# Kernel optimization log

Measured on AMD Instinct MI355X. Metric: run time of the kernel, lower is better.

## Reference

```python
import jax, jax.numpy as jnp
import numpy as np

T, B, I, H, L = 512, 256, 128, 256, 2

def _gru_layer(x, W_ih, W_hh, b_ih, b_hh):
    # x: [T, B, in], W_ih: [3H, in], W_hh: [3H, H], biases: [3H]
    # PyTorch gate order: r, z, n
    Hd = W_hh.shape[1]
    gi = jnp.einsum('tbi,gi->tbg', x, W_ih) + b_ih  # precompute input gates [T,B,3H]

    def step(h, gi_t):
        gh = h @ W_hh.T + b_hh
        i_r, i_z, i_n = jnp.split(gi_t, 3, axis=-1)
        h_r, h_z, h_n = jnp.split(gh, 3, axis=-1)
        r = jax.nn.sigmoid(i_r + h_r)
        z = jax.nn.sigmoid(i_z + h_z)
        n = jnp.tanh(i_n + r * h_n)
        h_new = (1.0 - z) * n + z * h
        return h_new, h_new

    h0 = jnp.zeros((x.shape[1], Hd), dtype=x.dtype)
    _, hs = jax.lax.scan(step, h0, gi)
    return hs  # [T, B, H]

def setup_inputs() -> dict:
    key = jax.random.key(0)
    ks = jax.random.split(key, 11)
    s = 1.0 / np.sqrt(H)
    u = lambda k, shp: jax.random.uniform(k, shp, jnp.float32, -s, s)
    return {
        'x': jax.random.normal(ks[0], (T, B, I), jnp.float32),
        'W_ih0': u(ks[1], (3 * H, I)),
        'W_hh0': u(ks[2], (3 * H, H)),
        'b_ih0': u(ks[3], (3 * H,)),
        'b_hh0': u(ks[4], (3 * H,)),
        'W_ih1': u(ks[5], (3 * H, H)),
        'W_hh1': u(ks[6], (3 * H, H)),
        'b_ih1': u(ks[7], (3 * H,)),
        'b_hh1': u(ks[8], (3 * H,)),
        'W_fc': u(ks[9], (H, H)),
        'b_fc': u(ks[10], (H,)),
    }

def reference(x, W_ih0, W_hh0, b_ih0, b_hh0, W_ih1, W_hh1, b_ih1, b_hh1, W_fc, b_fc):
    h1 = _gru_layer(x, W_ih0, W_hh0, b_ih0, b_hh0)   # [T,B,H]
    h2 = _gru_layer(h1, W_ih1, W_hh1, b_ih1, b_hh1)  # [T,B,H]
    last = h2[-1]                                    # [B,H] last timestep
    return last @ W_fc.T + b_fc
```

## Files before the change

### kernel.cpp

```cpp
#include <hip/hip_runtime.h>

#define TT 512
#define BB 256
#define II 128
#define HH 256

typedef __attribute__((ext_vector_type(8))) short short8;
typedef __attribute__((ext_vector_type(4))) float floatx4;
typedef __attribute__((ext_vector_type(4))) float fvec4;
typedef unsigned long long u64;

#define OFF_WIH0 0
#define OFF_WHH0 (OFF_WIH0 + 3 * HH * II)
#define OFF_WIH1 (OFF_WHH0 + 3 * HH * HH)
#define OFF_WHH1 (OFF_WIH1 + 3 * HH * HH)
#define W_TOTAL (OFF_WHH1 + 3 * HH * HH)
#define H1G_OFF W_TOTAL
#define H2G_OFF (H1G_OFF + 2 * BB * HH)
#define WS_SHORTS (H2G_OFF + 2 * BB * HH)
#define FLAGS_OFF_BYTES (WS_SHORTS * 2)
#define FLAG_STRIDE 32
#define HPARW (BB * HH / 4)

struct U64x2 { u64 lo, hi; };

__device__ __forceinline__ short f2bf(float f) {
  unsigned u = __builtin_bit_cast(unsigned, f);
  u = u + 0x7fffu + ((u >> 16) & 1u);
  return (short)(u >> 16);
}
__device__ __forceinline__ float fast_sigmoid(float x) {
  return __fdividef(1.0f, 1.0f + __expf(-x));
}
__device__ __forceinline__ float fast_tanh(float x) {
  return 1.0f - __fdividef(2.0f, 1.0f + __expf(2.0f * x));
}
__device__ __forceinline__ short8 cvt8(const float* __restrict__ p) {
  fvec4 lo = *(const fvec4*)p;
  fvec4 hi = *(const fvec4*)(p + 4);
  short8 r;
  r[0] = f2bf(lo[0]); r[1] = f2bf(lo[1]); r[2] = f2bf(lo[2]); r[3] = f2bf(lo[3]);
  r[4] = f2bf(hi[0]); r[5] = f2bf(hi[1]); r[6] = f2bf(hi[2]); r[7] = f2bf(hi[3]);
  return r;
}
__device__ __forceinline__ u64 ld_sc1(const u64* p) {
  return __hip_atomic_load(p, __ATOMIC_RELAXED, __HIP_MEMORY_SCOPE_AGENT);
}
__device__ __forceinline__ unsigned ld_flag(const unsigned* p) {
  return __hip_atomic_load(p, __ATOMIC_RELAXED, __HIP_MEMORY_SCOPE_AGENT);
}
__device__ __forceinline__ void st_flag(unsigned* p, unsigned v) {
  __hip_atomic_store(p, v, __ATOMIC_RELAXED, __HIP_MEMORY_SCOPE_AGENT);
}
__device__ __forceinline__ void st_h(unsigned short* p, unsigned short v) {
  __hip_atomic_store(p, v, __ATOMIC_RELAXED, __HIP_MEMORY_SCOPE_AGENT);
}
#define DRAIN_VMEM asm volatile("s_waitcnt vmcnt(0)" ::: "memory")

__global__ __launch_bounds__(256) void cvt_weights(
    const float* __restrict__ w0, const float* __restrict__ w1,
    const float* __restrict__ w2, const float* __restrict__ w3,
    short* __restrict__ out) {
  int i = blockIdx.x * 256 + threadIdx.x;
  if (i >= W_TOTAL) return;
  float v;
  if (i < OFF_WHH0)      v = w0[i - OFF_WIH0];
  else if (i < OFF_WIH1) v = w1[i - OFF_WHH0];
  else if (i < OFF_WHH1) v = w2[i - OFF_WIH1];
  else                   v = w3[i - OFF_WHH1];
  out[i] = f2bf(v);
}

__global__ __launch_bounds__(256) void init_state(unsigned* __restrict__ hz,
                                                  unsigned* __restrict__ flags) {
  int i = blockIdx.x * 256 + threadIdx.x;
  if (i < 2 * BB * HH) hz[i] = 0u;
  if (i < 32 * FLAG_STRIDE) flags[i] = 0u;
}

__global__ __launch_bounds__(64) void gru_sync(
    const float* __restrict__ x, const short* __restrict__ wb,
    const float* __restrict__ bih0, const float* __restrict__ bhh0,
    const float* __restrict__ bih1, const float* __restrict__ bhh1,
    const float* __restrict__ Wfc, const float* __restrict__ bfc,
    short* __restrict__ h1g, short* __restrict__ h2g,
    unsigned* __restrict__ flags, float* __restrict__ out) {
  const int lane = threadIdx.x;
  const int quad = lane >> 4;
  const int col = lane & 15;
  const int bid = blockIdx.x;
  const int layer = bid >> 8;
  const int bt = bid & 15;
  const int ht = (bid >> 4) & 15;
  const int j = ht * 16 + col;

  unsigned* h1fl = flags + bt * FLAG_STRIDE;
  unsigned* h2fl = flags + (16 + bt) * FLAG_STRIDE;
  unsigned* myfl = layer ? h2fl : h1fl;

  const short* wih = wb + (layer ? OFF_WIH1 : OFF_WIH0);
  const short* whh = wb + (layer ? OFF_WHH1 : OFF_WHH0);
  const int KI = layer ? HH : II;
  short8 wI0[8], wI1[8], wI2[8], wH0[8], wH1[8], wH2[8];
#pragma unroll
  for (int f = 0; f < 8; ++f) {
    if (f * 32 < KI) {
      wI0[f] = *(const short8*)(wih + (0 * HH + j) * KI + f * 32 + quad * 8);
      wI1[f] = *(const short8*)(wih + (1 * HH + j) * KI + f * 32 + quad * 8);
      wI2[f] = *(const short8*)(wih + (2 * HH + j) * KI + f * 32 + quad * 8);
    } else {
      wI0[f] = short8{0,0,0,0,0,0,0,0};
      wI1[f] = short8{0,0,0,0,0,0,0,0};
      wI2[f] = short8{0,0,0,0,0,0,0,0};
    }
    wH0[f] = *(const short8*)(whh + (0 * HH + j) * HH + f * 32 + quad * 8);
    wH1[f] = *(const short8*)(whh + (1 * HH + j) * HH + f * 32 + quad * 8);
    wH2[f] = *(const short8*)(whh + (2 * HH + j) * HH + f * 32 + quad * 8);
  }
  const float* bihL = layer ? bih1 : bih0;
  const float* bhhL = layer ? bhh1 : bhh0;
  const float bI0 = bihL[j] + bhhL[j];
  const float bI1 = bihL[HH + j] + bhhL[HH + j];
  const float bI2 = bihL[2 * HH + j];
  const float bH2 = bhhL[2 * HH + j];

  float hprev0 = 0.f, hprev1 = 0.f, hprev2 = 0.f, hprev3 = 0.f;

  const u64* h1w = (const u64*)h1g;
  const u64* h2w = (const u64*)h2g;
  const int rowW = (bt * 16 + col) * 64;

  for (int p = 0; p < TT; ++p) {
    short8 ax[4];
    if (layer == 0) {
      const float* xr = x + ((size_t)p * BB + bt * 16 + col) * II + quad * 8;
#pragma unroll
      for (int f = 0; f < 4; ++f) ax[f] = cvt8(xr + f * 32);
    }

    {
      unsigned tgt = 0;
      const unsigned* fp = h1fl;
      if (layer == 0) {
        if (lane < 16)      { tgt = (unsigned)p; fp = h1fl + lane; }
        else if (lane < 32) { tgt = (p >= 1) ? (unsigned)(p - 1) : 0u; fp = h2fl + (lane - 16); }
      } else {
        if (lane < 16)      { tgt = (unsigned)p; fp = h2fl + lane; }
        else if (lane < 32) { tgt = (unsigned)(p + 1); fp = h1fl + (lane - 16); }
      }
      if (layer == 1 || p > 0) {
        int guard = 0;
        for (;;) {
          unsigned v = ld_flag(fp);
          if (__all(v >= tgt) || ++guard > (1 << 20)) break;
        }
      }
    }

    short8 a1[8], a2[8];
    if (layer == 0) {
      const u64* s1 = h1w + ((p + 1) & 1) * HPARW + rowW;
#pragma unroll
      for (int f = 0; f < 8; ++f) {
        u64 lo = ld_sc1(s1 + f * 8 + quad * 2);
        u64 hi = ld_sc1(s1 + f * 8 + quad * 2 + 1);
        a1[f] = __builtin_bit_cast(short8, U64x2{lo, hi});
      }
    } else {
      const u64* s1 = h1w + (p & 1) * HPARW + rowW;
      const u64* s2 = h2w + ((p + 1) & 1) * HPARW + rowW;
#pragma unroll
      for (int f = 0; f < 8; ++f) {
        u64 lo = ld_sc1(s1 + f * 8 + quad * 2);
        u64 hi = ld_sc1(s1 + f * 8 + quad * 2 + 1);
        a1[f] = __builtin_bit_cast(short8, U64x2{lo, hi});
      }
#pragma unroll
      for (int f = 0; f < 8; ++f) {
        u64 lo = ld_sc1(s2 + f * 8 + quad * 2);
        u64 hi = ld_sc1(s2 + f * 8 + quad * 2 + 1);
        a2[f] = __builtin_bit_cast(short8, U64x2{lo, hi});
      }
    }

    floatx4 aR = floatx4{bI0, bI0, bI0, bI0};
    floatx4 aZ = floatx4{bI1, bI1, bI1, bI1};
    floatx4 aN = floatx4{bI2, bI2, bI2, bI2};
    floatx4 hN = floatx4{bH2, bH2, bH2, bH2};
    if (layer == 0) {
#pragma unroll
      for (int f = 0; f < 4; ++f) {
        aR = __builtin_amdgcn_mfma_f32_16x16x32_bf16(ax[f], wI0[f], aR, 0, 0, 0);
        aZ = __builtin_amdgcn_mfma_f32_16x16x32_bf16(ax[f], wI1[f], aZ, 0, 0, 0);
        aN = __builtin_amdgcn_mfma_f32_16x16x32_bf16(ax[f], wI2[f], aN, 0, 0, 0);
      }
#pragma unroll
      for (int f = 0; f < 8; ++f) {
        aR = __builtin_amdgcn_mfma_f32_16x16x32_bf16(a1[f], wH0[f], aR, 0, 0, 0);
        aZ = __builtin_amdgcn_mfma_f32_16x16x32_bf16(a1[f], wH1[f], aZ, 0, 0, 0);
        hN = __builtin_amdgcn_mfma_f32_16x16x32_bf16(a1[f], wH2[f], hN, 0, 0, 0);
      }
    } else {
#pragma unroll
      for (int f = 0; f < 8; ++f) {
        aR = __builtin_amdgcn_mfma_f32_16x16x32_bf16(a1[f], wI0[f], aR, 0, 0, 0);
        aZ = __builtin_amdgcn_mfma_f32_16x16x32_bf16(a1[f], wI1[f], aZ, 0, 0, 0);
        aN = __builtin_amdgcn_mfma_f32_16x16x32_bf16(a1[f], wI2[f], aN, 0, 0, 0);
      }
#pragma unroll
      for (int f = 0; f < 8; ++f) {
        aR = __builtin_amdgcn_mfma_f32_16x16x32_bf16(a2[f], wH0[f], aR, 0, 0, 0);
        aZ = __builtin_amdgcn_mfma_f32_16x16x32_bf16(a2[f], wH1[f], aZ, 0, 0, 0);
        hN = __builtin_amdgcn_mfma_f32_16x16x32_bf16(a2[f], wH2[f], hN, 0, 0, 0);
      }
    }

    short* hout = (layer ? h2g : h1g) + (p & 1) * BB * HH;
    unsigned short* dst = (unsigned short*)hout +
                          (size_t)(bt * 16 + quad * 4) * HH + j;
    {
      float r0 = fast_sigmoid(aR[0]), z0 = fast_sigmoid(aZ[0]);
      float n0 = fast_tanh(aN[0] + r0 * hN[0]);
      hprev0 = n0 + z0 * (hprev0 - n0);
      st_h(dst + 0 * HH, (unsigned short)f2bf(hprev0));
      float r1 = fast_sigmoid(aR[1]), z1 = fast_sigmoid(aZ[1]);
      float n1 = fast_tanh(aN[1] + r1 * hN[1]);
      hprev1 = n1 + z1 * (hprev1 - n1);
      st_h(dst + 1 * HH, (unsigned short)f2bf(hprev1));
      float r2 = fast_sigmoid(aR[2]), z2 = fast_sigmoid(aZ[2]);
      float n2 = fast_tanh(aN[2] + r2 * hN[2]);
      hprev2 = n2 + z2 * (hprev2 - n2);
      st_h(dst + 2 * HH, (unsigned short)f2bf(hprev2));
      float r3 = fast_sigmoid(aR[3]), z3 = fast_sigmoid(aZ[3]);
      float n3 = fast_tanh(aN[3] + r3 * hN[3]);
      hprev3 = n3 + z3 * (hprev3 - n3);
      st_h(dst + 3 * HH, (unsigned short)f2bf(hprev3));
    }
    DRAIN_VMEM;
    if (lane == 0) st_flag(myfl + ht, (unsigned)(p + 1));
  }

  if (layer == 1) {
    {
      int guard = 0;
      for (;;) {
        unsigned v = (lane < 16) ? ld_flag(h2fl + lane) : (unsigned)TT;
        if (__all(v >= (unsigned)TT) || ++guard > (1 << 20)) break;
      }
    }
    const u64* s2 = h2w + ((TT - 1) & 1) * HPARW + rowW;
    float bbv = bfc[j];
    floatx4 acc = floatx4{bbv, bbv, bbv, bbv};
#pragma unroll
    for (int f = 0; f < 8; ++f) {
      u64 lo = ld_sc1(s2 + f * 8 + quad * 2);
      u64 hi = ld_sc1(s2 + f * 8 + quad * 2 + 1);
      short8 a = __builtin_bit_cast(short8, U64x2{lo, hi});
      short8 bfrag = cvt8(Wfc + j * HH + f * 32 + quad * 8);
      acc = __builtin_amdgcn_mfma_f32_16x16x32_bf16(a, bfrag, acc, 0, 0, 0);
    }
#pragma unroll
    for (int i = 0; i < 4; ++i)
      out[(size_t)(bt * 16 + quad * 4 + i) * HH + j] = acc[i];
  }
}

extern "C" void kernel_launch(void* const* d_in, const int* in_sizes, int n_in,
                              void* d_out, int out_size, void* d_ws,
                              size_t ws_size, hipStream_t stream) {
  const float* x = (const float*)d_in[0];
  const float* Wih0 = (const float*)d_in[1];
  const float* Whh0 = (const float*)d_in[2];
  const float* bih0 = (const float*)d_in[3];
  const float* bhh0 = (const float*)d_in[4];
  const float* Wih1 = (const float*)d_in[5];
  const float* Whh1 = (const float*)d_in[6];
  const float* bih1 = (const float*)d_in[7];
  const float* bhh1 = (const float*)d_in[8];
  const float* Wfc = (const float*)d_in[9];
  const float* bfc = (const float*)d_in[10];

  short* wb = (short*)d_ws;
  short* h1g = wb + H1G_OFF;
  short* h2g = wb + H2G_OFF;
  unsigned* flags = (unsigned*)((char*)d_ws + FLAGS_OFF_BYTES);
  unsigned* hz = (unsigned*)(wb + H1G_OFF);

  cvt_weights<<<(W_TOTAL + 255) / 256, 256, 0, stream>>>(Wih0, Whh0, Wih1, Whh1, wb);
  init_state<<<(2 * BB * HH + 255) / 256, 256, 0, stream>>>(hz, flags);
  gru_sync<<<512, 64, 0, stream>>>(x, wb, bih0, bhh0, bih1, bhh1, Wfc, bfc,
                                   h1g, h2g, flags, (float*)d_out);
}
```

Baseline: 2.056 ms.

## Co-locate both GRU layers in one block with wavefront-skewed pipeline and shared flags

```diff
diff --git a/kernel.cpp b/kernel.cpp
--- a/kernel.cpp
+++ b/kernel.cpp
@@ -52,10 +52,9 @@
 __device__ __forceinline__ void st_flag(unsigned* p, unsigned v) {
   __hip_atomic_store(p, v, __ATOMIC_RELAXED, __HIP_MEMORY_SCOPE_AGENT);
 }
-__device__ __forceinline__ void st_h(unsigned short* p, unsigned short v) {
+__device__ __forceinline__ void st_u32(unsigned* p, unsigned v) {
   __hip_atomic_store(p, v, __ATOMIC_RELAXED, __HIP_MEMORY_SCOPE_AGENT);
 }
-#define DRAIN_VMEM asm volatile("s_waitcnt vmcnt(0)" ::: "memory")
 
 __global__ __launch_bounds__(256) void cvt_weights(
     const float* __restrict__ w0, const float* __restrict__ w1,
@@ -78,25 +77,24 @@
   if (i < 32 * FLAG_STRIDE) flags[i] = 0u;
 }
 
-__global__ __launch_bounds__(64) void gru_sync(
+__global__ __launch_bounds__(128) void gru_sync(
     const float* __restrict__ x, const short* __restrict__ wb,
     const float* __restrict__ bih0, const float* __restrict__ bhh0,
     const float* __restrict__ bih1, const float* __restrict__ bhh1,
     const float* __restrict__ Wfc, const float* __restrict__ bfc,
     short* __restrict__ h1g, short* __restrict__ h2g,
     unsigned* __restrict__ flags, float* __restrict__ out) {
-  const int lane = threadIdx.x;
+  const int tid = threadIdx.x;
+  const int lane = tid & 63;
+  const int w = tid >> 6;
   const int quad = lane >> 4;
   const int col = lane & 15;
-  const int bid = blockIdx.x;
-  const int layer = bid >> 8;
-  const int bt = bid & 15;
-  const int ht = (bid >> 4) & 15;
+  const int bt = blockIdx.x & 15;
+  const int ht = blockIdx.x >> 4;
+  const int layer = w;
   const int j = ht * 16 + col;
 
-  unsigned* h1fl = flags + bt * FLAG_STRIDE;
-  unsigned* h2fl = flags + (16 + bt) * FLAG_STRIDE;
-  unsigned* myfl = layer ? h2fl : h1fl;
+  unsigned* fl = flags + bt * FLAG_STRIDE;
 
   const short* wih = wb + (layer ? OFF_WIH1 : OFF_WIH0);
   const short* whh = wb + (layer ? OFF_WHH1 : OFF_WHH0);
@@ -130,35 +128,26 @@
   const u64* h2w = (const u64*)h2g;
   const int rowW = (bt * 16 + col) * 64;
 
-  for (int p = 0; p < TT; ++p) {
+  for (int p = 0; p <= TT; ++p) {
     short8 ax[4];
-    if (layer == 0) {
+    if (w == 0 && p < TT) {
       const float* xr = x + ((size_t)p * BB + bt * 16 + col) * II + quad * 8;
 #pragma unroll
       for (int f = 0; f < 4; ++f) ax[f] = cvt8(xr + f * 32);
     }
 
+    if (p > 0) {
+      const unsigned tgt = (unsigned)p;
+      int guard = 0;
+      for (;;) {
+        unsigned v = (lane < 16) ? ld_flag(fl + lane) : tgt;
+        if (__all(v >= tgt) || ++guard > (1 << 20)) break;
+        __builtin_amdgcn_s_sleep(1);
+      }
+    }
+
+    short8 a1[8], a2[8];
     {
-      unsigned tgt = 0;
-      const unsigned* fp = h1fl;
-      if (layer == 0) {
-        if (lane < 16)      { tgt = (unsigned)p; fp = h1fl + lane; }
-        else if (lane < 32) { tgt = (p >= 1) ? (unsigned)(p - 1) : 0u; fp = h2fl + (lane - 16); }
-      } else {
-        if (lane < 16)      { tgt = (unsigned)p; fp = h2fl + lane; }
-        else if (lane < 32) { tgt = (unsigned)(p + 1); fp = h1fl + (lane - 16); }
-      }
-      if (layer == 1 || p > 0) {
-        int guard = 0;
-        for (;;) {
-          unsigned v = ld_flag(fp);
-          if (__all(v >= tgt) || ++guard > (1 << 20)) break;
-        }
-      }
-    }
-
-    short8 a1[8], a2[8];
-    if (layer == 0) {
       const u64* s1 = h1w + ((p + 1) & 1) * HPARW + rowW;
 #pragma unroll
       for (int f = 0; f < 8; ++f) {
@@ -166,20 +155,14 @@
         u64 hi = ld_sc1(s1 + f * 8 + quad * 2 + 1);
         a1[f] = __builtin_bit_cast(short8, U64x2{lo, hi});
       }
-    } else {
-      const u64* s1 = h1w + (p & 1) * HPARW + rowW;
-      const u64* s2 = h2w + ((p + 1) & 1) * HPARW + rowW;
-#pragma unroll
-      for (int f = 0; f < 8; ++f) {
-        u64 lo = ld_sc1(s1 + f * 8 + quad * 2);
-        u64 hi = ld_sc1(s1 + f * 8 + quad * 2 + 1);
-        a1[f] = __builtin_bit_cast(short8, U64x2{lo, hi});
-      }
-#pragma unroll
-      for (int f = 0; f < 8; ++f) {
-        u64 lo = ld_sc1(s2 + f * 8 + quad * 2);
-        u64 hi = ld_sc1(s2 + f * 8 + quad * 2 + 1);
-        a2[f] = __builtin_bit_cast(short8, U64x2{lo, hi});
+      if (w == 1) {
+        const u64* s2 = h2w + (p & 1) * HPARW + rowW;
+#pragma unroll
+        for (int f = 0; f < 8; ++f) {
+          u64 lo = ld_sc1(s2 + f * 8 + quad * 2);
+          u64 hi = ld_sc1(s2 + f * 8 + quad * 2 + 1);
+          a2[f] = __builtin_bit_cast(short8, U64x2{lo, hi});
+        }
       }
     }
 
@@ -187,66 +170,83 @@
     floatx4 aZ = floatx4{bI1, bI1, bI1, bI1};
     floatx4 aN = floatx4{bI2, bI2, bI2, bI2};
     floatx4 hN = floatx4{bH2, bH2, bH2, bH2};
-    if (layer == 0) {
-#pragma unroll
-      for (int f = 0; f < 4; ++f) {
-        aR = __builtin_amdgcn_mfma_f32_16x16x32_bf16(ax[f], wI0[f], aR, 0, 0, 0);
-        aZ = __builtin_amdgcn_mfma_f32_16x16x32_bf16(ax[f], wI1[f], aZ, 0, 0, 0);
-        aN = __builtin_amdgcn_mfma_f32_16x16x32_bf16(ax[f], wI2[f], aN, 0, 0, 0);
-      }
-#pragma unroll
-      for (int f = 0; f < 8; ++f) {
-        aR = __builtin_amdgcn_mfma_f32_16x16x32_bf16(a1[f], wH0[f], aR, 0, 0, 0);
-        aZ = __builtin_amdgcn_mfma_f32_16x16x32_bf16(a1[f], wH1[f], aZ, 0, 0, 0);
-        hN = __builtin_amdgcn_mfma_f32_16x16x32_bf16(a1[f], wH2[f], hN, 0, 0, 0);
+    if (w == 0) {
+      if (p < TT) {
+#pragma unroll
+        for (int f = 0; f < 4; ++f) {
+          aR = __builtin_amdgcn_mfma_f32_16x16x32_bf16(ax[f], wI0[f], aR, 0, 0, 0);
+          aZ = __builtin_amdgcn_mfma_f32_16x16x32_bf16(ax[f], wI1[f], aZ, 0, 0, 0);
+          aN = __builtin_amdgcn_mfma_f32_16x16x32_bf16(ax[f], wI2[f], aN, 0, 0, 0);
+        }
+#pragma unroll
+        for (int f = 0; f < 8; ++f) {
+          aR = __builtin_amdgcn_mfma_f32_16x16x32_bf16(a1[f], wH0[f], aR, 0, 0, 0);
+          aZ = __builtin_amdgcn_mfma_f32_16x16x32_bf16(a1[f], wH1[f], aZ, 0, 0, 0);
+          hN = __builtin_amdgcn_mfma_f32_16x16x32_bf16(a1[f], wH2[f], hN, 0, 0, 0);
+        }
       }
     } else {
-#pragma unroll
-      for (int f = 0; f < 8; ++f) {
-        aR = __builtin_amdgcn_mfma_f32_16x16x32_bf16(a1[f], wI0[f], aR, 0, 0, 0);
-        aZ = __builtin_amdgcn_mfma_f32_16x16x32_bf16(a1[f], wI1[f], aZ, 0, 0, 0);
-        aN = __builtin_amdgcn_mfma_f32_16x16x32_bf16(a1[f], wI2[f], aN, 0, 0, 0);
-      }
-#pragma unroll
-      for (int f = 0; f < 8; ++f) {
-        aR = __builtin_amdgcn_mfma_f32_16x16x32_bf16(a2[f], wH0[f], aR, 0, 0, 0);
-        aZ = __builtin_amdgcn_mfma_f32_16x16x32_bf16(a2[f], wH1[f], aZ, 0, 0, 0);
-        hN = __builtin_amdgcn_mfma_f32_16x16x32_bf16(a2[f], wH2[f], hN, 0, 0, 0);
-      }
-    }
-
-    short* hout = (layer ? h2g : h1g) + (p & 1) * BB * HH;
-    unsigned short* dst = (unsigned short*)hout +
-                          (size_t)(bt * 16 + quad * 4) * HH + j;
-    {
+      if (p > 0) {
+#pragma unroll
+        for (int f = 0; f < 8; ++f) {
+          aR = __builtin_amdgcn_mfma_f32_16x16x32_bf16(a1[f], wI0[f], aR, 0, 0, 0);
+          aZ = __builtin_amdgcn_mfma_f32_16x16x32_bf16(a1[f], wI1[f], aZ, 0, 0, 0);
+          aN = __builtin_amdgcn_mfma_f32_16x16x32_bf16(a1[f], wI2[f], aN, 0, 0, 0);
+        }
+#pragma unroll
+        for (int f = 0; f < 8; ++f) {
+          aR = __builtin_amdgcn_mfma_f32_16x16x32_bf16(a2[f], wH0[f], aR, 0, 0, 0);
+          aZ = __builtin_amdgcn_mfma_f32_16x16x32_bf16(a2[f], wH1[f], aZ, 0, 0, 0);
+          hN = __builtin_amdgcn_mfma_f32_16x16x32_bf16(a2[f], wH2[f], hN, 0, 0, 0);
+        }
+      }
+    }
+
+    const bool doPub = (w == 0) ? (p < TT) : (p > 0);
+    if (doPub) {
       float r0 = fast_sigmoid(aR[0]), z0 = fast_sigmoid(aZ[0]);
       float n0 = fast_tanh(aN[0] + r0 * hN[0]);
       hprev0 = n0 + z0 * (hprev0 - n0);
-      st_h(dst + 0 * HH, (unsigned short)f2bf(hprev0));
       float r1 = fast_sigmoid(aR[1]), z1 = fast_sigmoid(aZ[1]);
       float n1 = fast_tanh(aN[1] + r1 * hN[1]);
       hprev1 = n1 + z1 * (hprev1 - n1);
-      st_h(dst + 1 * HH, (unsigned short)f2bf(hprev1));
       float r2 = fast_sigmoid(aR[2]), z2 = fast_sigmoid(aZ[2]);
       float n2 = fast_tanh(aN[2] + r2 * hN[2]);
       hprev2 = n2 + z2 * (hprev2 - n2);
-      st_h(dst + 2 * HH, (unsigned short)f2bf(hprev2));
       float r3 = fast_sigmoid(aR[3]), z3 = fast_sigmoid(aZ[3]);
       float n3 = fast_tanh(aN[3] + r3 * hN[3]);
       hprev3 = n3 + z3 * (hprev3 - n3);
-      st_h(dst + 3 * HH, (unsigned short)f2bf(hprev3));
-    }
-    DRAIN_VMEM;
-    if (lane == 0) st_flag(myfl + ht, (unsigned)(p + 1));
+
+      unsigned m0 = (unsigned)(unsigned short)f2bf(hprev0);
+      unsigned m1 = (unsigned)(unsigned short)f2bf(hprev1);
+      unsigned m2 = (unsigned)(unsigned short)f2bf(hprev2);
+      unsigned m3 = (unsigned)(unsigned short)f2bf(hprev3);
+      unsigned o0 = (unsigned)__shfl_xor((int)m0, 1);
+      unsigned o1 = (unsigned)__shfl_xor((int)m1, 1);
+      unsigned o2 = (unsigned)__shfl_xor((int)m2, 1);
+      unsigned o3 = (unsigned)__shfl_xor((int)m3, 1);
+      if (!(col & 1)) {
+        short* hout = (w == 0) ? (h1g + (p & 1) * BB * HH)
+                               : (h2g + ((p + 1) & 1) * BB * HH);
+        unsigned* db = (unsigned*)hout;
+        const int base = ((bt * 16 + quad * 4) * HH + j) >> 1;
+        st_u32(db + base + 0 * (HH / 2), m0 | (o0 << 16));
+        st_u32(db + base + 1 * (HH / 2), m1 | (o1 << 16));
+        st_u32(db + base + 2 * (HH / 2), m2 | (o2 << 16));
+        st_u32(db + base + 3 * (HH / 2), m3 | (o3 << 16));
+      }
+    }
+    __syncthreads();
+    if (tid == 0) st_flag(fl + ht, (unsigned)(p + 1));
   }
 
-  if (layer == 1) {
-    {
-      int guard = 0;
-      for (;;) {
-        unsigned v = (lane < 16) ? ld_flag(h2fl + lane) : (unsigned)TT;
-        if (__all(v >= (unsigned)TT) || ++guard > (1 << 20)) break;
-      }
+  if (w == 0) {
+    const unsigned tgt = (unsigned)(TT + 1);
+    int guard = 0;
+    for (;;) {
+      unsigned v = (lane < 16) ? ld_flag(fl + lane) : tgt;
+      if (__all(v >= tgt) || ++guard > (1 << 20)) break;
+      __builtin_amdgcn_s_sleep(1);
     }
     const u64* s2 = h2w + ((TT - 1) & 1) * HPARW + rowW;
     float bbv = bfc[j];
@@ -288,6 +288,6 @@
 
   cvt_weights<<<(W_TOTAL + 255) / 256, 256, 0, stream>>>(Wih0, Whh0, Wih1, Whh1, wb);
   init_state<<<(2 * BB * HH + 255) / 256, 256, 0, stream>>>(hz, flags);
-  gru_sync<<<512, 64, 0, stream>>>(x, wb, bih0, bhh0, bih1, bhh1, Wfc, bfc,
-                                   h1g, h2g, flags, (float*)d_out);
-}
+  gru_sync<<<256, 128, 0, stream>>>(x, wb, bih0, bhh0, bih1, bhh1, Wfc, bfc,
+                                    h1g, h2g, flags, (float*)d_out);
+}
```

Measured after the change: 1.946 ms. -5.4%, faster.
